# Optimization experiments

Measured on AMD Instinct MI355X. Metric: run time of the kernel, lower is better.

## Reference

```python
import jax, jax.numpy as jnp
import numpy as np

N = 50000      # num nodes
E = 800000     # num edges
F_IN = 256     # num_features
H = 256        # hidden_dim
C = 40         # num_classes
ALPHA = 0.5    # fixed mixing coefficient (learn_alpha=False)


def setup_inputs() -> dict:
    key = jax.random.key(0)
    ks = jax.random.split(key, 16)
    inp = {
        "x": jax.random.normal(ks[0], (N, F_IN), dtype=jnp.float32),
        "edge_index": jax.random.randint(ks[1], (2, E), 0, N, dtype=jnp.int64),
    }
    dims = [(F_IN, H), (H, H), (H, C)]
    ki = 2
    for i, (din, dout) in enumerate(dims, start=1):
        inp[f"w_s{i}"] = jax.random.normal(ks[ki], (dout, din), dtype=jnp.float32) * 0.02; ki += 1
        inp[f"b_s{i}"] = jnp.zeros((dout,), dtype=jnp.float32)
        inp[f"w_d{i}"] = jax.random.normal(ks[ki], (dout, din), dtype=jnp.float32) * 0.02; ki += 1
        inp[f"b_d{i}"] = jnp.zeros((dout,), dtype=jnp.float32)
    return inp


def _dir_edge_weight(row, col, dtype):
    # directed norm: D_out^{-1/2} A D_in^{-1/2}; per-edge weight
    ones = jnp.ones(row.shape, dtype)
    deg_out = jax.ops.segment_sum(ones, row, num_segments=N)
    deg_in = jax.ops.segment_sum(ones, col, num_segments=N)
    inv_out = jnp.where(deg_out > 0, jax.lax.rsqrt(jnp.maximum(deg_out, 1e-12)), 0.0)
    inv_in = jnp.where(deg_in > 0, jax.lax.rsqrt(jnp.maximum(deg_in, 1e-12)), 0.0)
    return inv_out[row] * inv_in[col]  # [E]; same weight serves adj and adj^T


def reference(x, edge_index, w_s1, b_s1, w_d1, b_d1, w_s2, b_s2, w_d2, b_d2, w_s3, b_s3, w_d3, b_d3):
    row, col = edge_index[0], edge_index[1]
    ew = _dir_edge_weight(row, col, x.dtype)

    def dir_gcn(h, ws, bs, wd, bd):
        # adj_norm @ h : out[r] += ew * h[c]
        agg = jax.ops.segment_sum(ew[:, None] * h[col], row, num_segments=N)
        # adj_t_norm @ h : out[c] += ew * h[r]  (same edge weights, transposed aggregation)
        agg_t = jax.ops.segment_sum(ew[:, None] * h[row], col, num_segments=N)
        return ALPHA * (agg @ ws.T + bs) + (1.0 - ALPHA) * (agg_t @ wd.T + bd)

    h = jax.nn.relu(dir_gcn(x, w_s1, b_s1, w_d1, b_d1))   # dropout p=0 -> no-op
    h = jax.nn.relu(dir_gcn(h, w_s2, b_s2, w_d2, b_d2))
    h = dir_gcn(h, w_s3, b_s3, w_d3, b_d3)
    return jax.nn.log_softmax(h, axis=1)
```

## Files before the change

### kernel.cpp

```cpp
#include <hip/hip_runtime.h>
#include <math.h>

#define FDIM 256
#define CDIM 40
#define ZPAD 64
#define NPAD_TO 128
#define NPART 16
#define BLKS_PER_PART 64
#define CNT_BLKS (NPART * BLKS_PER_PART * 2)

typedef __attribute__((ext_vector_type(8))) __bf16 bf16x8;
typedef __attribute__((ext_vector_type(4))) float f32x4;
typedef __attribute__((ext_vector_type(8))) ushort u16x8;
typedef __attribute__((ext_vector_type(4))) ushort u16x4;

static inline int cdiv(int a, int b) { return (a + b - 1) / b; }

__device__ __forceinline__ float b2f(ushort u) { return __uint_as_float(((unsigned)u) << 16); }
__device__ __forceinline__ ushort f2bf(float f) {
    unsigned u = __float_as_uint(f);
    unsigned r = (u + 0x7FFFu + ((u >> 16) & 1u)) >> 16;
    return (ushort)r;
}
__device__ __forceinline__ unsigned char f2fp8(float f) {
    int p = __builtin_amdgcn_cvt_pk_fp8_f32(f, f, 0, false);
    return (unsigned char)(p & 0xff);
}

__device__ __forceinline__ void gl_lds16(const void* gsrc, void* ldst) {
    __builtin_amdgcn_global_load_lds((const __attribute__((address_space(1))) unsigned*)gsrc,
                                     (__attribute__((address_space(3))) unsigned*)ldst, 16, 0, 0);
}

#define ACC8(v, w)                                                      \
    {                                                                   \
        auto p0 = __builtin_amdgcn_cvt_pk_f32_fp8((v).x, false);        \
        auto p1 = __builtin_amdgcn_cvt_pk_f32_fp8((v).x, true);         \
        auto p2 = __builtin_amdgcn_cvt_pk_f32_fp8((v).y, false);        \
        auto p3 = __builtin_amdgcn_cvt_pk_f32_fp8((v).y, true);         \
        a[0] += (w) * p0[0]; a[1] += (w) * p0[1];                       \
        a[2] += (w) * p1[0]; a[3] += (w) * p1[1];                       \
        a[4] += (w) * p2[0]; a[5] += (w) * p2[1];                       \
        a[6] += (w) * p3[0]; a[7] += (w) * p3[1];                       \
    }

__global__ __launch_bounds__(256) void k_pro2(const int* __restrict__ row,
                                              const int* __restrict__ col,
                                              int* __restrict__ cnt_r,
                                              int* __restrict__ cnt_c, int E, int N,
                                              const float* __restrict__ x, int n4,
                                              const float* __restrict__ s1, const float* __restrict__ d1,
                                              const float* __restrict__ s2, const float* __restrict__ d2,
                                              const float* __restrict__ s3, const float* __restrict__ d3,
                                              unsigned char* __restrict__ xb8,
                                              ushort* __restrict__ wb) {
    int bid = blockIdx.x;
    if (bid < CNT_BLKS) {
        int part = bid & (NPART - 1);
        int dir = (bid >> 4) & 1;
        int blk = bid >> 5;
        int rpp = (N + NPART - 1) / NPART;
        int lo = part * rpp;
        int hi = lo + rpp;
        if (hi > N) hi = N;
        const int* key = dir ? col : row;
        int* cnt = dir ? cnt_c : cnt_r;
        for (int e = blk * 256 + threadIdx.x; e < E; e += BLKS_PER_PART * 256) {
            int k = key[e];
            if (k >= lo && k < hi) atomicAdd(&cnt[k], 1);
        }
        return;
    }
    int i = (bid - CNT_BLKS) * 256 + threadIdx.x;
    if (i < n4) {
        float4 v = ((const float4*)x)[i];
        uchar4 o;
        o.x = f2fp8(v.x); o.y = f2fp8(v.y); o.z = f2fp8(v.z); o.w = f2fp8(v.w);
        ((uchar4*)xb8)[i] = o;
        return;
    }
    int o = i - n4;
    const int BIG = 256 * 256;
    const int SM = 64 * 256;
    if (o >= 4 * BIG + 2 * SM) return;
    float v;
    if (o < BIG) v = s1[o];
    else if (o < 2 * BIG) v = d1[o - BIG];
    else if (o < 3 * BIG) v = s2[o - 2 * BIG];
    else if (o < 4 * BIG) v = d2[o - 3 * BIG];
    else {
        int oo = o - 4 * BIG;
        const float* src = (oo < SM) ? s3 : d3;
        oo = (oo < SM) ? oo : oo - SM;
        int r = oo >> 8;
        v = (r < CDIM) ? src[(r << 8) + (oo & 255)] : 0.0f;
    }
    wb[o] = f2bf(v);
}

__global__ __launch_bounds__(256) void k_scan1(const int* __restrict__ cnt_r,
                                               const int* __restrict__ cnt_c,
                                               int* __restrict__ rptr,
                                               int* __restrict__ cptr,
                                               int* __restrict__ bsum, int n) {
    const int* cnt = blockIdx.y ? cnt_c : cnt_r;
    int* ptr = blockIdx.y ? cptr : rptr;
    __shared__ int s[256];
    int t = threadIdx.x;
    int i = blockIdx.x * 256 + t;
    int v = (i < n) ? cnt[i] : 0;
    s[t] = v;
    __syncthreads();
    for (int off = 1; off < 256; off <<= 1) {
        int u = (t >= off) ? s[t - off] : 0;
        __syncthreads();
        s[t] += u;
        __syncthreads();
    }
    if (i < n) ptr[i] = s[t] - v;
    if (t == 255) bsum[blockIdx.y * 256 + blockIdx.x] = s[255];
}

__global__ __launch_bounds__(256) void k_scan2(int* __restrict__ bsum, int nb) {
    int* b = bsum + blockIdx.x * 256;
    __shared__ int s[256];
    int t = threadIdx.x;
    int v = (t < nb) ? b[t] : 0;
    s[t] = v;
    __syncthreads();
    for (int off = 1; off < 256; off <<= 1) {
        int u = (t >= off) ? s[t - off] : 0;
        __syncthreads();
        s[t] += u;
        __syncthreads();
    }
    if (t < nb) b[t] = s[t] - v;
}

__global__ __launch_bounds__(256) void k_scan3(int* __restrict__ rptr,
                                               int* __restrict__ cptr,
                                               const int* __restrict__ bsum,
                                               const int* __restrict__ cnt_r,
                                               const int* __restrict__ cnt_c,
                                               float* __restrict__ inv_out,
                                               float* __restrict__ inv_in,
                                               int n, int total) {
    int i = blockIdx.x * 256 + threadIdx.x;
    if (blockIdx.y == 0) {
        if (i < n) {
            rptr[i] += bsum[blockIdx.x];
            int cv = cnt_r[i];
            inv_out[i] = cv > 0 ? rsqrtf((float)cv) : 0.0f;
        }
        if (blockIdx.x == 0 && threadIdx.x == 0) rptr[n] = total;
    } else {
        if (i < n) {
            cptr[i] += bsum[256 + blockIdx.x];
            int cv = cnt_c[i];
            inv_in[i] = cv > 0 ? rsqrtf((float)cv) : 0.0f;
        }
        if (blockIdx.x == 0 && threadIdx.x == 0) cptr[n] = total;
    }
}

__global__ __launch_bounds__(256) void k_fillp(const int* __restrict__ row,
                                               const int* __restrict__ col,
                                               const int* __restrict__ rptr,
                                               const int* __restrict__ cptr,
                                               int* __restrict__ fr, int* __restrict__ fc,
                                               int* __restrict__ nbr_r,
                                               int* __restrict__ nbr_c,
                                               int E, int N) {
    int part = blockIdx.x & (NPART - 1);
    int blk = blockIdx.x >> 4;
    int rpp = (N + NPART - 1) / NPART;
    int lo = part * rpp;
    int hi = lo + rpp;
    if (hi > N) hi = N;
    const int* key = blockIdx.y ? col : row;
    const int* val = blockIdx.y ? row : col;
    const int* ptr = blockIdx.y ? cptr : rptr;
    int* f = blockIdx.y ? fc : fr;
    int* nbr = blockIdx.y ? nbr_c : nbr_r;
    for (int e = blk * 256 + threadIdx.x; e < E; e += BLKS_PER_PART * 256) {
        int k = key[e];
        if (k >= lo && k < hi) {
            int p = ptr[k] + atomicAdd(&f[k], 1);
            nbr[p] = val[e];
        }
    }
}

__global__ __launch_bounds__(256) void k_gather_f8(const unsigned char* __restrict__ h8,
                                                   const int* __restrict__ rptr,
                                                   const int* __restrict__ nbr_r,
                                                   const int* __restrict__ cptr,
                                                   const int* __restrict__ nbr_c,
                                                   const float* __restrict__ inv_out,
                                                   const float* __restrict__ inv_in,
                                                   ushort* __restrict__ agg,
                                                   ushort* __restrict__ aggt, int N) {
    int wv = threadIdx.x >> 6, lane = threadIdx.x & 63;
    int half = lane >> 5, l32 = lane & 31;
    int n = blockIdx.x * 4 + wv;
    if (n >= N) return;
    const int* ptr;
    const int* nbr;
    const float* invt;
    float fac;
    ushort* out;
    if (blockIdx.y == 0) { ptr = rptr; nbr = nbr_r; invt = inv_in; fac = inv_out[n]; out = agg; }
    else                 { ptr = cptr; nbr = nbr_c; invt = inv_out; fac = inv_in[n]; out = aggt; }
    int s = ptr[n], t = ptr[n + 1];
    float a[8] = {};
    for (int base = s; base < t; base += 64) {
        int cnt = t - base;
        if (cnt > 64) cnt = 64;
        int idx = 0;
        float ww = 0.f;
        if (lane < cnt) {
            idx = nbr[base + lane];
            ww = invt[idx];
        }
        for (int i = 0; i < cnt; i += 8) {
            int n0 = i + half, n1 = i + 2 + half, n2 = i + 4 + half, n3 = i + 6 + half;
            int c0 = __shfl(idx, n0, 64); float w0 = __shfl(ww, n0, 64);
            int c1 = __shfl(idx, n1, 64); float w1 = __shfl(ww, n1, 64);
            int c2 = __shfl(idx, n2, 64); float w2 = __shfl(ww, n2, 64);
            int c3 = __shfl(idx, n3, 64); float w3 = __shfl(ww, n3, 64);
            uint2 v0 = ((const uint2*)(h8 + (size_t)c0 * FDIM))[l32];
            uint2 v1 = ((const uint2*)(h8 + (size_t)c1 * FDIM))[l32];
            uint2 v2 = ((const uint2*)(h8 + (size_t)c2 * FDIM))[l32];
            uint2 v3 = ((const uint2*)(h8 + (size_t)c3 * FDIM))[l32];
            ACC8(v0, w0);
            ACC8(v1, w1);
            ACC8(v2, w2);
            ACC8(v3, w3);
        }
    }
#pragma unroll
    for (int j = 0; j < 8; ++j) a[j] += __shfl_xor(a[j], 32, 64);
    if (half == 0) {
        u16x8 o;
#pragma unroll
        for (int j = 0; j < 8; ++j) o[j] = f2bf(a[j] * fac);
        ((u16x8*)(out + (size_t)n * FDIM))[l32] = o;
    }
}

__global__ __launch_bounds__(256) void k_gemm12(const ushort* __restrict__ Ab,
                                                const ushort* __restrict__ Atb,
                                                const ushort* __restrict__ Wsb,
                                                const ushort* __restrict__ Wdb,
                                                const float* __restrict__ bs,
                                                const float* __restrict__ bd,
                                                ushort* __restrict__ outH,
                                                unsigned char* __restrict__ out8) {
    __shared__ char smA[8192];
    __shared__ char smAt[8192];
    __shared__ char smWs[16384];
    __shared__ char smWd[16384];

    const int tid = threadIdx.x;
    const int wv = tid >> 6, lane = tid & 63;
    const int n0 = blockIdx.x * 64;
    const int j0 = blockIdx.y * 128;

    const char* Abase = (const char*)Ab;
    const char* Atbase = (const char*)Atb;
    const char* Wsbase = (const char*)Wsb;
    const char* Wdbase = (const char*)Wdb;

    f32x4 accS[8] = {};
    f32x4 accD[8] = {};

    for (int k0 = 0; k0 < FDIM; k0 += 64) {
#pragma unroll
        for (int it = 0; it < 2; ++it) {
            int si = it * 256 + tid;
            int r = si >> 3, sl = si & 7;
            int gs = sl ^ (r & 7);
            size_t goff = (size_t)(n0 + r) * (FDIM * 2) + k0 * 2 + gs * 16;
            gl_lds16(Abase + goff, smA + si * 16);
            gl_lds16(Atbase + goff, smAt + si * 16);
        }
#pragma unroll
        for (int it = 0; it < 4; ++it) {
            int si = it * 256 + tid;
            int r = si >> 3, sl = si & 7;
            int gs = sl ^ (r & 7);
            size_t goff = (size_t)(j0 + r) * (FDIM * 2) + k0 * 2 + gs * 16;
            gl_lds16(Wsbase + goff, smWs + si * 16);
            gl_lds16(Wdbase + goff, smWd + si * 16);
        }
        __syncthreads();
#pragma unroll
        for (int kh = 0; kh < 2; ++kh) {
            int rA = wv * 16 + (lane & 15);
            int sA = (kh * 4 + (lane >> 4)) ^ (rA & 7);
            bf16x8 aS = *(const bf16x8*)(smA + rA * 128 + sA * 16);
            bf16x8 aT = *(const bf16x8*)(smAt + rA * 128 + sA * 16);
#pragma unroll
            for (int ni = 0; ni < 8; ++ni) {
                int rB = ni * 16 + (lane & 15);
                int sB = (kh * 4 + (lane >> 4)) ^ (rB & 7);
                bf16x8 bSv = *(const bf16x8*)(smWs + rB * 128 + sB * 16);
                bf16x8 bDv = *(const bf16x8*)(smWd + rB * 128 + sB * 16);
                accS[ni] = __builtin_amdgcn_mfma_f32_16x16x32_bf16(aS, bSv, accS[ni], 0, 0, 0);
                accD[ni] = __builtin_amdgcn_mfma_f32_16x16x32_bf16(aT, bDv, accD[ni], 0, 0, 0);
            }
        }
        __syncthreads();
    }

#pragma unroll
    for (int ni = 0; ni < 8; ++ni) {
        int j = j0 + ni * 16 + (lane & 15);
        float bsv = bs[j], bdv = bd[j];
#pragma unroll
        for (int r = 0; r < 4; ++r) {
            int n = n0 + wv * 16 + (lane >> 4) * 4 + r;
            float v = 0.5f * (accS[ni][r] + bsv) + 0.5f * (accD[ni][r] + bdv);
            v = fmaxf(v, 0.0f);
            if (out8) out8[(size_t)n * FDIM + j] = f2fp8(v);
            else outH[(size_t)n * FDIM + j] = f2bf(v);
        }
    }
}

__global__ __launch_bounds__(256) void k_gemm3(const ushort* __restrict__ Hb,
                                               const ushort* __restrict__ Wsb,
                                               const ushort* __restrict__ Wdb,
                                               unsigned char* __restrict__ zs8,
                                               unsigned char* __restrict__ zd8) {
    __shared__ char smA[16384];
    __shared__ char smWs[8192];
    __shared__ char smWd[8192];

    const int tid = threadIdx.x;
    const int wv = tid >> 6, lane = tid & 63;
    const int n0 = blockIdx.x * 128;

    const char* Abase = (const char*)Hb;
    const char* Wsbase = (const char*)Wsb;
    const char* Wdbase = (const char*)Wdb;

    f32x4 accS[2][4] = {};
    f32x4 accD[2][4] = {};

    for (int k0 = 0; k0 < FDIM; k0 += 64) {
#pragma unroll
        for (int it = 0; it < 4; ++it) {
            int si = (wv * 4 + it) * 64 + lane;
            int r = si >> 3, sl = si & 7;
            int gs = sl ^ (r & 7);
            size_t goff = (size_t)(n0 + r) * (FDIM * 2) + k0 * 2 + gs * 16;
            gl_lds16(Abase + goff, smA + si * 16);
        }
#pragma unroll
        for (int it = 0; it < 2; ++it) {
            int si = (wv * 2 + it) * 64 + lane;
            int r = si >> 3, sl = si & 7;
            int gs = sl ^ (r & 7);
            size_t goff = (size_t)r * (FDIM * 2) + k0 * 2 + gs * 16;
            gl_lds16(Wsbase + goff, smWs + si * 16);
            gl_lds16(Wdbase + goff, smWd + si * 16);
        }
        __syncthreads();
#pragma unroll
        for (int kh = 0; kh < 2; ++kh) {
            bf16x8 aS[2], bS[4], bD[4];
#pragma unroll
            for (int mi = 0; mi < 2; ++mi) {
                int r = wv * 32 + mi * 16 + (lane & 15);
                int off = r * 128 + (((kh * 4 + (lane >> 4)) ^ (r & 7)) * 16);
                aS[mi] = *(const bf16x8*)(smA + off);
            }
#pragma unroll
            for (int ni = 0; ni < 4; ++ni) {
                int r = ni * 16 + (lane & 15);
                int off = r * 128 + (((kh * 4 + (lane >> 4)) ^ (r & 7)) * 16);
                bS[ni] = *(const bf16x8*)(smWs + off);
                bD[ni] = *(const bf16x8*)(smWd + off);
            }
#pragma unroll
            for (int mi = 0; mi < 2; ++mi)
#pragma unroll
                for (int ni = 0; ni < 4; ++ni) {
                    accS[mi][ni] = __builtin_amdgcn_mfma_f32_16x16x32_bf16(aS[mi], bS[ni], accS[mi][ni], 0, 0, 0);
                    accD[mi][ni] = __builtin_amdgcn_mfma_f32_16x16x32_bf16(aS[mi], bD[ni], accD[mi][ni], 0, 0, 0);
                }
        }
        __syncthreads();
    }

#pragma unroll
    for (int mi = 0; mi < 2; ++mi)
#pragma unroll
        for (int ni = 0; ni < 4; ++ni) {
            int j = ni * 16 + (lane & 15);
            f32x4 cs = accS[mi][ni], cd = accD[mi][ni];
#pragma unroll
            for (int r = 0; r < 4; ++r) {
                int n = n0 + wv * 32 + mi * 16 + (lane >> 4) * 4 + r;
                zs8[(size_t)n * ZPAD + j] = f2fp8(cs[r]);
                zd8[(size_t)n * ZPAD + j] = f2fp8(cd[r]);
            }
        }
}

__global__ __launch_bounds__(256) void k_l3(const unsigned char* __restrict__ zs8,
                                            const unsigned char* __restrict__ zd8,
                                            const int* __restrict__ rptr,
                                            const int* __restrict__ nbr_r,
                                            const int* __restrict__ cptr,
                                            const int* __restrict__ nbr_c,
                                            const float* __restrict__ inv_out,
                                            const float* __restrict__ inv_in,
                                            const float* __restrict__ bs,
                                            const float* __restrict__ bd,
                                            float* __restrict__ out, int N) {
    int wv = threadIdx.x >> 6, lane = threadIdx.x & 63;
    int grp = lane >> 4, sl = lane & 15;
    int n = blockIdx.x * 4 + wv;
    if (n >= N) return;
    float acc[2][4] = {};

#pragma unroll
    for (int dir = 0; dir < 2; ++dir) {
        const int* ptr = dir == 0 ? rptr : cptr;
        const int* nbr = dir == 0 ? nbr_r : nbr_c;
        const float* invt = dir == 0 ? inv_in : inv_out;
        const unsigned char* zb = dir == 0 ? zs8 : zd8;
        int s = ptr[n], t = ptr[n + 1];
        for (int base = s; base < t; base += 64) {
            int cnt = t - base;
            if (cnt > 64) cnt = 64;
            int idx = 0;
            float ww = 0.f;
            if (lane < cnt) {
                idx = nbr[base + lane];
                ww = invt[idx];
            }
            for (int i = 0; i < cnt; i += 8) {
                int n0 = i + grp, n1 = i + 4 + grp;
                int c0 = __shfl(idx, n0, 64); float w0 = __shfl(ww, n0, 64);
                int c1 = __shfl(idx, n1, 64); float w1 = __shfl(ww, n1, 64);
                unsigned v0 = ((const unsigned*)(zb + (size_t)c0 * ZPAD))[sl];
                unsigned v1 = ((const unsigned*)(zb + (size_t)c1 * ZPAD))[sl];
                auto p00 = __builtin_amdgcn_cvt_pk_f32_fp8(v0, false);
                auto p01 = __builtin_amdgcn_cvt_pk_f32_fp8(v0, true);
                auto p10 = __builtin_amdgcn_cvt_pk_f32_fp8(v1, false);
                auto p11 = __builtin_amdgcn_cvt_pk_f32_fp8(v1, true);
                acc[dir][0] += w0 * p00[0] + w1 * p10[0];
                acc[dir][1] += w0 * p00[1] + w1 * p10[1];
                acc[dir][2] += w0 * p01[0] + w1 * p11[0];
                acc[dir][3] += w0 * p01[1] + w1 * p11[1];
            }
        }
    }

    float fac0 = 0.5f * inv_out[n], fac1 = 0.5f * inv_in[n];
    float a[4];
#pragma unroll
    for (int j = 0; j < 4; ++j) {
        a[j] = fac0 * acc[0][j] + fac1 * acc[1][j];
        a[j] += __shfl_xor(a[j], 16, 64);
        a[j] += __shfl_xor(a[j], 32, 64);
    }
    float val[4];
#pragma unroll
    for (int j = 0; j < 4; ++j) {
        int c = 4 * sl + j;
        val[j] = (c < CDIM) ? a[j] + 0.5f * (bs[c] + bd[c]) : -INFINITY;
    }
    float m = fmaxf(fmaxf(val[0], val[1]), fmaxf(val[2], val[3]));
    for (int off = 1; off < 16; off <<= 1) m = fmaxf(m, __shfl_xor(m, off, 64));
    float ex = 0.f;
#pragma unroll
    for (int j = 0; j < 4; ++j) ex += (4 * sl + j < CDIM) ? expf(val[j] - m) : 0.f;
    for (int off = 1; off < 16; off <<= 1) ex += __shfl_xor(ex, off, 64);
    float lse = logf(ex);
    if (grp == 0 && sl < 10) {
        float4 o;
        o.x = val[0] - m - lse;
        o.y = val[1] - m - lse;
        o.z = val[2] - m - lse;
        o.w = val[3] - m - lse;
        ((float4*)(out + (size_t)n * CDIM))[sl] = o;
    }
}

extern "C" void kernel_launch(void* const* d_in, const int* in_sizes, int n_in,
                              void* d_out, int out_size, void* d_ws, size_t ws_size,
                              hipStream_t stream) {
    const int N = in_sizes[0] / FDIM;
    const int E = in_sizes[1] / 2;
    const int NP = cdiv(N, NPAD_TO) * NPAD_TO;

    const float* x = (const float*)d_in[0];
    const int* ei = (const int*)d_in[1];
    const int* row = ei;
    const int* col = ei + E;
    const float* ws1 = (const float*)d_in[2];
    const float* bs1 = (const float*)d_in[3];
    const float* wd1 = (const float*)d_in[4];
    const float* bd1 = (const float*)d_in[5];
    const float* ws2 = (const float*)d_in[6];
    const float* bs2 = (const float*)d_in[7];
    const float* wd2 = (const float*)d_in[8];
    const float* bd2 = (const float*)d_in[9];
    const float* ws3 = (const float*)d_in[10];
    const float* bs3 = (const float*)d_in[11];
    const float* wd3 = (const float*)d_in[12];
    const float* bd3 = (const float*)d_in[13];
    float* out = (float*)d_out;

    char* base = (char*)d_ws;
    int* cnt_r = (int*)base;        base += sizeof(int) * N;
    int* cnt_c = (int*)base;        base += sizeof(int) * N;
    int* fr = (int*)base;           base += sizeof(int) * N;
    int* fc = (int*)base;           base += sizeof(int) * N;
    int* rptr = (int*)base;         base += sizeof(int) * (N + 1);
    int* cptr = (int*)base;         base += sizeof(int) * (N + 1);
    int* bsum = (int*)base;         base += sizeof(int) * 512;
    float* inv_out = (float*)base;  base += sizeof(float) * N;
    float* inv_in = (float*)base;   base += sizeof(float) * N;
    base = (char*)(((size_t)base + 15) & ~(size_t)15);
    int* nbr_r = (int*)base;        base += sizeof(int) * E;
    int* nbr_c = (int*)base;        base += sizeof(int) * E;
    base = (char*)(((size_t)base + 255) & ~(size_t)255);
    unsigned char* xb8 = (unsigned char*)base;  base += (size_t)NP * FDIM;
    base = (char*)(((size_t)base + 255) & ~(size_t)255);
    unsigned char* hb8 = (unsigned char*)base;  base += (size_t)NP * FDIM;
    base = (char*)(((size_t)base + 255) & ~(size_t)255);
    ushort* hb = (ushort*)base;     base += sizeof(ushort) * (size_t)NP * FDIM;
    ushort* aggb = (ushort*)base;   base += sizeof(ushort) * (size_t)NP * FDIM;
    ushort* aggtb = (ushort*)base;  base += sizeof(ushort) * (size_t)NP * FDIM;
    ushort* wbuf = (ushort*)base;   base += sizeof(ushort) * (4 * 65536 + 2 * 16384);
    unsigned char* zs8 = (unsigned char*)aggb;
    unsigned char* zd8 = (unsigned char*)aggtb;

    ushort* w1s = wbuf;
    ushort* w1d = wbuf + 65536;
    ushort* w2s = wbuf + 2 * 65536;
    ushort* w2d = wbuf + 3 * 65536;
    ushort* w3s = wbuf + 4 * 65536;
    ushort* w3d = wbuf + 4 * 65536 + 16384;

    const int nb = cdiv(N, 256);
    const int n4 = N * FDIM / 4;
    const int wn = 4 * 65536 + 2 * 16384;

    hipMemsetAsync(cnt_r, 0, sizeof(int) * 4 * (size_t)N, stream);
    k_pro2<<<CNT_BLKS + cdiv(n4 + wn, 256), 256, 0, stream>>>(row, col, cnt_r, cnt_c, E, N,
                                                              x, n4, ws1, wd1, ws2, wd2, ws3, wd3,
                                                              xb8, wbuf);
    k_scan1<<<dim3(nb, 2), 256, 0, stream>>>(cnt_r, cnt_c, rptr, cptr, bsum, N);
    k_scan2<<<2, 256, 0, stream>>>(bsum, nb);
    k_scan3<<<dim3(nb, 2), 256, 0, stream>>>(rptr, cptr, bsum, cnt_r, cnt_c, inv_out, inv_in, N, E);
    k_fillp<<<dim3(NPART * BLKS_PER_PART, 2), 256, 0, stream>>>(row, col, rptr, cptr,
                                                                fr, fc, nbr_r, nbr_c, E, N);

    dim3 ggrid(cdiv(N, 4), 2);
    dim3 ggemm(NP / 64, 2);
    dim3 ggemm3(NP / 128, 1);

    k_gather_f8<<<ggrid, 256, 0, stream>>>(xb8, rptr, nbr_r, cptr, nbr_c, inv_out, inv_in, aggb, aggtb, N);
    k_gemm12<<<ggemm, 256, 0, stream>>>(aggb, aggtb, w1s, w1d, bs1, bd1, nullptr, hb8);

    k_gather_f8<<<ggrid, 256, 0, stream>>>(hb8, rptr, nbr_r, cptr, nbr_c, inv_out, inv_in, aggb, aggtb, N);
    k_gemm12<<<ggemm, 256, 0, stream>>>(aggb, aggtb, w2s, w2d, bs2, bd2, hb, nullptr);

    k_gemm3<<<ggemm3, 256, 0, stream>>>(hb, w3s, w3d, zs8, zd8);
    k_l3<<<cdiv(N, 4), 256, 0, stream>>>(zs8, zd8, rptr, nbr_r, cptr, nbr_c, inv_out, inv_in,
                                         bs3, bd3, out, N);
}
```

Before: 389.6 us.

## Build CSR with per-block LDS histograms instead of global atomics

```diff
diff --git a/kernel.cpp b/kernel.cpp
--- a/kernel.cpp
+++ b/kernel.cpp
@@ -5,9 +5,10 @@
 #define CDIM 40
 #define ZPAD 64
 #define NPAD_TO 128
-#define NPART 16
-#define BLKS_PER_PART 64
-#define CNT_BLKS (NPART * BLKS_PER_PART * 2)
+#define NPART 8
+#define NBLK 32
+#define CNTB (2 * NPART * NBLK)
+#define RSZMAX 6400
 
 typedef __attribute__((ext_vector_type(8))) __bf16 bf16x8;
 typedef __attribute__((ext_vector_type(4))) float f32x4;
@@ -44,34 +45,43 @@
         a[6] += (w) * p3[0]; a[7] += (w) * p3[1];                       \
     }
 
-__global__ __launch_bounds__(256) void k_pro2(const int* __restrict__ row,
-                                              const int* __restrict__ col,
-                                              int* __restrict__ cnt_r,
-                                              int* __restrict__ cnt_c, int E, int N,
-                                              const float* __restrict__ x, int n4,
-                                              const float* __restrict__ s1, const float* __restrict__ d1,
-                                              const float* __restrict__ s2, const float* __restrict__ d2,
-                                              const float* __restrict__ s3, const float* __restrict__ d3,
-                                              unsigned char* __restrict__ xb8,
-                                              ushort* __restrict__ wb) {
+__global__ __launch_bounds__(256) void k_cnt(const int* __restrict__ row,
+                                             const int* __restrict__ col,
+                                             int* __restrict__ blkcnt, int E, int N,
+                                             const float* __restrict__ x, int n4,
+                                             const float* __restrict__ s1, const float* __restrict__ d1,
+                                             const float* __restrict__ s2, const float* __restrict__ d2,
+                                             const float* __restrict__ s3, const float* __restrict__ d3,
+                                             unsigned char* __restrict__ xb8,
+                                             ushort* __restrict__ wb) {
     int bid = blockIdx.x;
-    if (bid < CNT_BLKS) {
-        int part = bid & (NPART - 1);
-        int dir = (bid >> 4) & 1;
-        int blk = bid >> 5;
+    if (bid < CNTB) {
+        int dir = bid >> 8;
+        int rest = bid & 255;
+        int part = rest >> 5;
+        int blk = rest & 31;
         int rpp = (N + NPART - 1) / NPART;
         int lo = part * rpp;
         int hi = lo + rpp;
         if (hi > N) hi = N;
+        __shared__ unsigned hist[RSZMAX];
+        for (int i = threadIdx.x; i < rpp; i += 256) hist[i] = 0;
+        __syncthreads();
         const int* key = dir ? col : row;
-        int* cnt = dir ? cnt_c : cnt_r;
-        for (int e = blk * 256 + threadIdx.x; e < E; e += BLKS_PER_PART * 256) {
+        int per = (E + NBLK - 1) / NBLK;
+        int e0 = blk * per;
+        int e1 = e0 + per;
+        if (e1 > E) e1 = E;
+        for (int e = e0 + threadIdx.x; e < e1; e += 256) {
             int k = key[e];
-            if (k >= lo && k < hi) atomicAdd(&cnt[k], 1);
-        }
+            if (k >= lo && k < hi) atomicAdd(&hist[k - lo], 1u);
+        }
+        __syncthreads();
+        int* dst = blkcnt + ((size_t)(dir * NPART + part) * NBLK + blk) * rpp;
+        for (int i = threadIdx.x; i < rpp; i += 256) dst[i] = (int)hist[i];
         return;
     }
-    int i = (bid - CNT_BLKS) * 256 + threadIdx.x;
+    int i = (bid - CNTB) * 256 + threadIdx.x;
     if (i < n4) {
         float4 v = ((const float4*)x)[i];
         uchar4 o;
@@ -98,6 +108,29 @@
     wb[o] = f2bf(v);
 }
 
+__global__ __launch_bounds__(256) void k_red(int* __restrict__ blkcnt,
+                                             int* __restrict__ cnt_r,
+                                             int* __restrict__ cnt_c,
+                                             float* __restrict__ inv_out,
+                                             float* __restrict__ inv_in, int N) {
+    int dir = blockIdx.y;
+    int n = blockIdx.x * 256 + threadIdx.x;
+    if (n >= N) return;
+    int rpp = (N + NPART - 1) / NPART;
+    int part = n / rpp, i = n - part * rpp;
+    int* p = blkcnt + ((size_t)(dir * NPART + part) * NBLK) * rpp + i;
+    int s = 0;
+#pragma unroll
+    for (int b = 0; b < NBLK; ++b) {
+        int v = p[(size_t)b * rpp];
+        p[(size_t)b * rpp] = s;
+        s += v;
+    }
+    float iv = s > 0 ? rsqrtf((float)s) : 0.0f;
+    if (dir == 0) { cnt_r[n] = s; inv_out[n] = iv; }
+    else          { cnt_c[n] = s; inv_in[n] = iv; }
+}
+
 __global__ __launch_bounds__(256) void k_scan1(const int* __restrict__ cnt_r,
                                                const int* __restrict__ cnt_c,
                                                int* __restrict__ rptr,
@@ -140,53 +173,47 @@
 __global__ __launch_bounds__(256) void k_scan3(int* __restrict__ rptr,
                                                int* __restrict__ cptr,
                                                const int* __restrict__ bsum,
-                                               const int* __restrict__ cnt_r,
-                                               const int* __restrict__ cnt_c,
-                                               float* __restrict__ inv_out,
-                                               float* __restrict__ inv_in,
                                                int n, int total) {
+    int* ptr = blockIdx.y ? cptr : rptr;
     int i = blockIdx.x * 256 + threadIdx.x;
-    if (blockIdx.y == 0) {
-        if (i < n) {
-            rptr[i] += bsum[blockIdx.x];
-            int cv = cnt_r[i];
-            inv_out[i] = cv > 0 ? rsqrtf((float)cv) : 0.0f;
-        }
-        if (blockIdx.x == 0 && threadIdx.x == 0) rptr[n] = total;
-    } else {
-        if (i < n) {
-            cptr[i] += bsum[256 + blockIdx.x];
-            int cv = cnt_c[i];
-            inv_in[i] = cv > 0 ? rsqrtf((float)cv) : 0.0f;
-        }
-        if (blockIdx.x == 0 && threadIdx.x == 0) cptr[n] = total;
-    }
-}
-
-__global__ __launch_bounds__(256) void k_fillp(const int* __restrict__ row,
+    if (i < n) ptr[i] += bsum[blockIdx.y * 256 + blockIdx.x];
+    if (blockIdx.x == 0 && threadIdx.x == 0) ptr[n] = total;
+}
+
+__global__ __launch_bounds__(256) void k_fill2(const int* __restrict__ row,
                                                const int* __restrict__ col,
                                                const int* __restrict__ rptr,
                                                const int* __restrict__ cptr,
-                                               int* __restrict__ fr, int* __restrict__ fc,
+                                               const int* __restrict__ blkoff,
                                                int* __restrict__ nbr_r,
                                                int* __restrict__ nbr_c,
                                                int E, int N) {
-    int part = blockIdx.x & (NPART - 1);
-    int blk = blockIdx.x >> 4;
+    int bid = blockIdx.x;
+    int part = bid & 7;
+    int rest = bid >> 3;
+    int dir = rest >> 5;
+    int blk = rest & 31;
     int rpp = (N + NPART - 1) / NPART;
     int lo = part * rpp;
     int hi = lo + rpp;
     if (hi > N) hi = N;
-    const int* key = blockIdx.y ? col : row;
-    const int* val = blockIdx.y ? row : col;
-    const int* ptr = blockIdx.y ? cptr : rptr;
-    int* f = blockIdx.y ? fc : fr;
-    int* nbr = blockIdx.y ? nbr_c : nbr_r;
-    for (int e = blk * 256 + threadIdx.x; e < E; e += BLKS_PER_PART * 256) {
+    __shared__ unsigned used[RSZMAX];
+    for (int i = threadIdx.x; i < rpp; i += 256) used[i] = 0;
+    __syncthreads();
+    const int* key = dir ? col : row;
+    const int* val = dir ? row : col;
+    const int* ptr = dir ? cptr : rptr;
+    int* nbr = dir ? nbr_c : nbr_r;
+    const int* off = blkoff + ((size_t)(dir * NPART + part) * NBLK + blk) * rpp;
+    int per = (E + NBLK - 1) / NBLK;
+    int e0 = blk * per;
+    int e1 = e0 + per;
+    if (e1 > E) e1 = E;
+    for (int e = e0 + threadIdx.x; e < e1; e += 256) {
         int k = key[e];
         if (k >= lo && k < hi) {
-            int p = ptr[k] + atomicAdd(&f[k], 1);
-            nbr[p] = val[e];
+            int u = (int)atomicAdd(&used[k - lo], 1u);
+            nbr[ptr[k] + off[k - lo] + u] = val[e];
         }
     }
 }
@@ -497,6 +524,7 @@
     const int N = in_sizes[0] / FDIM;
     const int E = in_sizes[1] / 2;
     const int NP = cdiv(N, NPAD_TO) * NPAD_TO;
+    const int rpp = cdiv(N, NPART);
 
     const float* x = (const float*)d_in[0];
     const int* ei = (const int*)d_in[1];
@@ -519,14 +547,13 @@
     char* base = (char*)d_ws;
     int* cnt_r = (int*)base;        base += sizeof(int) * N;
     int* cnt_c = (int*)base;        base += sizeof(int) * N;
-    int* fr = (int*)base;           base += sizeof(int) * N;
-    int* fc = (int*)base;           base += sizeof(int) * N;
     int* rptr = (int*)base;         base += sizeof(int) * (N + 1);
     int* cptr = (int*)base;         base += sizeof(int) * (N + 1);
     int* bsum = (int*)base;         base += sizeof(int) * 512;
     float* inv_out = (float*)base;  base += sizeof(float) * N;
     float* inv_in = (float*)base;   base += sizeof(float) * N;
     base = (char*)(((size_t)base + 15) & ~(size_t)15);
+    int* blkcnt = (int*)base;       base += sizeof(int) * (size_t)2 * NPART * NBLK * rpp;
     int* nbr_r = (int*)base;        base += sizeof(int) * E;
     int* nbr_c = (int*)base;        base += sizeof(int) * E;
     base = (char*)(((size_t)base + 255) & ~(size_t)255);
@@ -552,15 +579,14 @@
     const int n4 = N * FDIM / 4;
     const int wn = 4 * 65536 + 2 * 16384;
 
-    hipMemsetAsync(cnt_r, 0, sizeof(int) * 4 * (size_t)N, stream);
-    k_pro2<<<CNT_BLKS + cdiv(n4 + wn, 256), 256, 0, stream>>>(row, col, cnt_r, cnt_c, E, N,
-                                                              x, n4, ws1, wd1, ws2, wd2, ws3, wd3,
-                                                              xb8, wbuf);
+    k_cnt<<<CNTB + cdiv(n4 + wn, 256), 256, 0, stream>>>(row, col, blkcnt, E, N,
+                                                         x, n4, ws1, wd1, ws2, wd2, ws3, wd3,
+                                                         xb8, wbuf);
+    k_red<<<dim3(nb, 2), 256, 0, stream>>>(blkcnt, cnt_r, cnt_c, inv_out, inv_in, N);
     k_scan1<<<dim3(nb, 2), 256, 0, stream>>>(cnt_r, cnt_c, rptr, cptr, bsum, N);
     k_scan2<<<2, 256, 0, stream>>>(bsum, nb);
-    k_scan3<<<dim3(nb, 2), 256, 0, stream>>>(rptr, cptr, bsum, cnt_r, cnt_c, inv_out, inv_in, N, E);
-    k_fillp<<<dim3(NPART * BLKS_PER_PART, 2), 256, 0, stream>>>(row, col, rptr, cptr,
-                                                                fr, fc, nbr_r, nbr_c, E, N);
+    k_scan3<<<dim3(nb, 2), 256, 0, stream>>>(rptr, cptr, bsum, N, E);
+    k_fill2<<<CNTB, 256, 0, stream>>>(row, col, rptr, cptr, blkcnt, nbr_r, nbr_c, E, N);
 
     dim3 ggrid(cdiv(N, 4), 2);
     dim3 ggemm(NP / 64, 2);
```

Measured after the change: 347.3 us. 10.9% less time.
